# Optimization experiments

Hardware: AMD Instinct MI355X
Metric: run time of the kernel (lower is better)

Reference implementation:

```python
import jax, jax.numpy as jnp
import numpy as np

N, E, D, H, L = 50000, 800000, 256, 256, 40
HIDLAYERS = 3
NEG_SLOPE = 0.2  # PyG GATConv default leaky_relu slope


def _add_self_loops(edge_index, n):
    loop = jnp.arange(n, dtype=edge_index.dtype)
    src = jnp.concatenate([edge_index[0], loop])
    dst = jnp.concatenate([edge_index[1], loop])
    return src, dst


def gcn_conv(x, edge_index, W, b, n):
    # PyG GCNConv: add self-loops, symmetric deg^-1/2 normalization, linear, scatter-add
    src, dst = _add_self_loops(edge_index, n)
    ones = jnp.ones(src.shape[0], dtype=x.dtype)
    deg = jax.ops.segment_sum(ones, dst, num_segments=n)
    dinv = jnp.where(deg > 0, jax.lax.rsqrt(deg), 0.0)
    h = x @ W  # [n, out]
    norm = dinv[src] * dinv[dst]  # [E+n]
    out = jax.ops.segment_sum(h[src] * norm[:, None], dst, num_segments=n)
    return out + b


def gat_conv(x, edge_index, W, a_src, a_dst, b, n):
    # PyG GATConv (heads=1): add self-loops, e = leaky_relu(a_src.h_j + a_dst.h_i),
    # softmax over incoming edges per destination node, weighted scatter-add
    src, dst = _add_self_loops(edge_index, n)
    h = x @ W  # [n, H]
    al_src = h @ a_src  # [n]
    al_dst = h @ a_dst  # [n]
    e = jax.nn.leaky_relu(al_src[src] + al_dst[dst], NEG_SLOPE)  # [E+n]
    # numerically stable segment softmax over dst (self-loops => no empty segments)
    m = jax.ops.segment_max(e, dst, num_segments=n)
    ex = jnp.exp(e - m[dst])
    z = jax.ops.segment_sum(ex, dst, num_segments=n)
    alpha = ex / z[dst]
    out = jax.ops.segment_sum(h[src] * alpha[:, None], dst, num_segments=n)
    return out + b


def setup_inputs() -> dict:
    key = jax.random.key(0)
    ks = jax.random.split(key, 8)
    s = 0.05
    return {
        "x": jax.random.normal(ks[0], (N, D), jnp.float32),
        "edge_index": jax.random.randint(ks[1], (2, E), 0, N, dtype=jnp.int64),
        "W1": jax.random.normal(ks[2], (D, H), jnp.float32) * s,
        "b1": jnp.zeros((H,), jnp.float32),
        "Wg": jax.random.normal(ks[3], (H, H), jnp.float32) * s,
        "a_src": jax.random.normal(ks[4], (H,), jnp.float32) * s,
        "a_dst": jax.random.normal(ks[5], (H,), jnp.float32) * s,
        "bg": jnp.zeros((H,), jnp.float32),
        "W2": jax.random.normal(ks[6], (H, L), jnp.float32) * s,
        "b2": jnp.zeros((L,), jnp.float32),
    }


def reference(x, edge_index, W1, b1, Wg, a_src, a_dst, bg, W2, b2):
    n = x.shape[0]
    # feature standardization (torch .std is unbiased, ddof=1)
    x = (x - x.mean(axis=0, keepdims=True)) / x.std(axis=0, keepdims=True, ddof=1)
    x = jax.nn.relu(gcn_conv(x, edge_index, W1, b1, n))  # dropout = identity (eval)
    for _ in range(HIDLAYERS - 1):
        x = jax.nn.relu(gat_conv(x, edge_index, Wg, a_src, a_dst, bg, n))
    x = gcn_conv(x, edge_index, W2, b2, n)
    return jax.nn.log_softmax(x, axis=1)
```

## Files before the change

### kernel.cpp

```cpp
#include <hip/hip_runtime.h>
#include <math.h>

#define DD 256
#define LL 40
#define NSLOPE 0.2f
#define SCHUNK 1024

typedef unsigned short u16;
typedef unsigned int uint;
typedef __attribute__((ext_vector_type(8))) short short8;
typedef __attribute__((ext_vector_type(4))) float f32x4;

__device__ __forceinline__ float bf2f(u16 v) { return __uint_as_float(((uint)v) << 16); }
__device__ __forceinline__ u16 f2bf(float f) {
  uint u = __float_as_uint(f);
  return (u16)((u + 0x7fff + ((u >> 16) & 1)) >> 16);
}
__device__ __forceinline__ void acc8(float* a, uint4 v) {
  a[0] += __uint_as_float(v.x << 16);
  a[1] += __uint_as_float(v.x & 0xffff0000u);
  a[2] += __uint_as_float(v.y << 16);
  a[3] += __uint_as_float(v.y & 0xffff0000u);
  a[4] += __uint_as_float(v.z << 16);
  a[5] += __uint_as_float(v.z & 0xffff0000u);
  a[6] += __uint_as_float(v.w << 16);
  a[7] += __uint_as_float(v.w & 0xffff0000u);
}
__device__ __forceinline__ void wacc8(float* a, uint4 v, float w) {
  a[0] += w * __uint_as_float(v.x << 16);
  a[1] += w * __uint_as_float(v.x & 0xffff0000u);
  a[2] += w * __uint_as_float(v.y << 16);
  a[3] += w * __uint_as_float(v.y & 0xffff0000u);
  a[4] += w * __uint_as_float(v.z << 16);
  a[5] += w * __uint_as_float(v.z & 0xffff0000u);
  a[6] += w * __uint_as_float(v.w << 16);
  a[7] += w * __uint_as_float(v.w & 0xffff0000u);
}

__global__ __launch_bounds__(256) void k_colstats(const float* __restrict__ x, float* __restrict__ csum,
                                                  float* __restrict__ csq, int n, int rowsPerBlk) {
  int col = threadIdx.x;
  int r0 = blockIdx.x * rowsPerBlk;
  int r1 = min(r0 + rowsPerBlk, n);
  float s0 = 0.f, s1 = 0.f, s2 = 0.f, s3 = 0.f;
  float q0 = 0.f, q1 = 0.f, q2 = 0.f, q3 = 0.f;
  const float* xc = x + col;
  int r = r0;
  for (; r + 8 <= r1; r += 8) {
    float v0 = xc[(size_t)(r + 0) * DD];
    float v1 = xc[(size_t)(r + 1) * DD];
    float v2 = xc[(size_t)(r + 2) * DD];
    float v3 = xc[(size_t)(r + 3) * DD];
    float v4 = xc[(size_t)(r + 4) * DD];
    float v5 = xc[(size_t)(r + 5) * DD];
    float v6 = xc[(size_t)(r + 6) * DD];
    float v7 = xc[(size_t)(r + 7) * DD];
    s0 += v0; q0 = fmaf(v0, v0, q0);
    s1 += v1; q1 = fmaf(v1, v1, q1);
    s2 += v2; q2 = fmaf(v2, v2, q2);
    s3 += v3; q3 = fmaf(v3, v3, q3);
    s0 += v4; q0 = fmaf(v4, v4, q0);
    s1 += v5; q1 = fmaf(v5, v5, q1);
    s2 += v6; q2 = fmaf(v6, v6, q2);
    s3 += v7; q3 = fmaf(v7, v7, q3);
  }
  for (; r < r1; ++r) {
    float v = xc[(size_t)r * DD];
    s0 += v; q0 = fmaf(v, v, q0);
  }
  atomicAdd(&csum[col], (s0 + s1) + (s2 + s3));
  atomicAdd(&csq[col], (q0 + q1) + (q2 + q3));
}

__global__ void k_finalize_stats(const float* __restrict__ csum, const float* __restrict__ csq,
                                 float* __restrict__ mean, float* __restrict__ rstd, int n) {
  int j = threadIdx.x;
  float s = csum[j], q = csq[j];
  float m = s / (float)n;
  float var = (q - s * m) / (float)(n - 1);
  mean[j] = m;
  rstd[j] = 1.0f / sqrtf(var);
}

__global__ void k_standardize(const float* __restrict__ x, const float* __restrict__ mean,
                              const float* __restrict__ rstd, u16* __restrict__ xs, int total4) {
  int i = blockIdx.x * blockDim.x + threadIdx.x;
  if (i >= total4) return;
  int c4 = i & (DD / 4 - 1);
  float4 v = ((const float4*)x)[i];
  float4 m = ((const float4*)mean)[c4];
  float4 r = ((const float4*)rstd)[c4];
  uint2 o;
  o.x = (uint)f2bf((v.x - m.x) * r.x) | ((uint)f2bf((v.y - m.y) * r.y) << 16);
  o.y = (uint)f2bf((v.z - m.z) * r.z) | ((uint)f2bf((v.w - m.w) * r.w) << 16);
  ((uint2*)xs)[i] = o;
}

__global__ void k_convWt(const float* __restrict__ W, u16* __restrict__ Wt, int K, int N) {
  int k = blockIdx.x;
  for (int nn = threadIdx.x; nn < N; nn += blockDim.x)
    Wt[(size_t)nn * K + k] = f2bf(W[(size_t)k * N + nn]);
}

__global__ void k_count_deg(const int* __restrict__ edst, int E, int* __restrict__ degi) {
  int i = blockIdx.x * blockDim.x + threadIdx.x;
  if (i < E) atomicAdd(&degi[edst[i]], 1);
}

__global__ __launch_bounds__(256) void k_blocksum(const int* __restrict__ degi, int* __restrict__ bsum, int n) {
  int b = blockIdx.x, tid = threadIdx.x;
  int base = b * SCHUNK;
  int end = min(base + SCHUNK, n);
  int s = 0;
  for (int i = base + tid; i < end; i += 256) s += degi[i] + 1;
  __shared__ int ws[4];
  #pragma unroll
  for (int off = 32; off >= 1; off >>= 1) s += __shfl_down(s, off);
  if ((tid & 63) == 0) ws[tid >> 6] = s;
  __syncthreads();
  if (tid == 0) bsum[b] = ws[0] + ws[1] + ws[2] + ws[3];
}

__global__ void k_scan_bsums(int* __restrict__ bsum, int nb) {
  int lane = threadIdx.x;
  int orig = (lane < nb) ? bsum[lane] : 0;
  int v = orig;
  #pragma unroll
  for (int off = 1; off < 64; off <<= 1) {
    int t = __shfl_up(v, off);
    if (lane >= off) v += t;
  }
  if (lane < nb) bsum[lane] = v - orig;
}

__global__ __launch_bounds__(256) void k_rowptr_write(const int* __restrict__ degi, const int* __restrict__ bsum,
                                                      int* __restrict__ rowptr, int* __restrict__ cursor,
                                                      float* __restrict__ dinv, int n) {
  int b = blockIdx.x, tid = threadIdx.x;
  int base = b * SCHUNK + tid * 4;
  int d[4];
  int t = 0;
  #pragma unroll
  for (int j = 0; j < 4; ++j) {
    int i = base + j;
    d[j] = (i < n) ? degi[i] + 1 : 0;
    t += d[j];
  }
  __shared__ int sc[256];
  sc[tid] = t;
  __syncthreads();
  for (int off = 1; off < 256; off <<= 1) {
    int v = 0;
    if (tid >= off) v = sc[tid - off];
    __syncthreads();
    if (tid >= off) sc[tid] += v;
    __syncthreads();
  }
  int run = bsum[b] + sc[tid] - t;
  #pragma unroll
  for (int j = 0; j < 4; ++j) {
    int i = base + j;
    if (i < n) {
      rowptr[i] = run;
      cursor[i] = run;
      dinv[i] = rsqrtf((float)d[j]);
      run += d[j];
      if (i == n - 1) rowptr[n] = run;
    }
  }
}

__global__ void k_scatter(const int* __restrict__ esrc, const int* __restrict__ edst, int E,
                          int* __restrict__ cursor, int* __restrict__ csrsrc) {
  int i = blockIdx.x * blockDim.x + threadIdx.x;
  if (i < E) {
    int d = edst[i];
    int p = atomicAdd(&cursor[d], 1);
    csrsrc[p] = esrc[i];
  }
}

__global__ void k_selfloop(const int* __restrict__ rowptr, int* __restrict__ csrsrc, int n) {
  int i = blockIdx.x * blockDim.x + threadIdx.x;
  if (i < n) csrsrc[rowptr[i + 1] - 1] = i;
}

__global__ __launch_bounds__(256) void k_mfma_gemm128(const u16* __restrict__ A, const u16* __restrict__ Bt,
                                                      u16* __restrict__ C, int M, int N, int K,
                                                      const float* __restrict__ rowScale) {
  __shared__ u16 As[128 * 40];
  __shared__ u16 Bs[128 * 40];
  int tid = threadIdx.x;
  int wave = tid >> 6, lane = tid & 63, quad = lane >> 4, l16 = lane & 15;
  int rowBase = blockIdx.y * 128, colBase = blockIdx.x * 128;
  f32x4 acc[2][8] = {};
  for (int k0 = 0; k0 < K; k0 += 32) {
    #pragma unroll
    for (int i = 0; i < 2; ++i) {
      int ch = tid + i * 256;
      int r = ch >> 2, cc = (ch & 3) * 8;
      int gr = min(rowBase + r, M - 1);
      *(uint4*)&As[r * 40 + cc] = *(const uint4*)(A + (size_t)gr * K + k0 + cc);
      *(uint4*)&Bs[r * 40 + cc] = *(const uint4*)(Bt + (size_t)(colBase + r) * K + k0 + cc);
    }
    __syncthreads();
    short8 af0 = *(const short8*)&As[(wave * 32 + l16) * 40 + quad * 8];
    short8 af1 = *(const short8*)&As[(wave * 32 + 16 + l16) * 40 + quad * 8];
    #pragma unroll
    for (int j = 0; j < 8; ++j) {
      short8 bf = *(const short8*)&Bs[(j * 16 + l16) * 40 + quad * 8];
      acc[0][j] = __builtin_amdgcn_mfma_f32_16x16x32_bf16(af0, bf, acc[0][j], 0, 0, 0);
      acc[1][j] = __builtin_amdgcn_mfma_f32_16x16x32_bf16(af1, bf, acc[1][j], 0, 0, 0);
    }
    __syncthreads();
  }
  #pragma unroll
  for (int i = 0; i < 2; ++i) {
    #pragma unroll
    for (int r = 0; r < 4; ++r) {
      int gr = rowBase + wave * 32 + i * 16 + quad * 4 + r;
      if (gr >= M) continue;
      float sc = rowScale ? rowScale[gr] : 1.0f;
      #pragma unroll
      for (int j = 0; j < 8; ++j) {
        int gc = colBase + j * 16 + l16;
        C[(size_t)gr * N + gc] = f2bf(acc[i][j][r] * sc);
      }
    }
  }
}

__global__ __launch_bounds__(256) void k_mfma_gemm(const u16* __restrict__ A, const u16* __restrict__ Bt,
                                                   u16* __restrict__ C, int M, int N, int K,
                                                   const float* __restrict__ rowScale) {
  __shared__ u16 As[128 * 40];
  __shared__ u16 Bs[64 * 40];
  int tid = threadIdx.x;
  int wave = tid >> 6, lane = tid & 63, quad = lane >> 4, l16 = lane & 15;
  int rowBase = blockIdx.y * 128, colBase = blockIdx.x * 64;
  f32x4 acc[2][4] = {};
  for (int k0 = 0; k0 < K; k0 += 32) {
    #pragma unroll
    for (int i = 0; i < 2; ++i) {
      int ch = tid + i * 256;
      int r = ch >> 2, cc = (ch & 3) * 8;
      int gr = rowBase + r;
      uint4 v = make_uint4(0, 0, 0, 0);
      if (gr < M) v = *(const uint4*)(A + (size_t)gr * K + k0 + cc);
      *(uint4*)&As[r * 40 + cc] = v;
    }
    {
      int r = tid >> 2, cc = (tid & 3) * 8;
      int gn = colBase + r;
      uint4 v = make_uint4(0, 0, 0, 0);
      if (gn < N) v = *(const uint4*)(Bt + (size_t)gn * K + k0 + cc);
      *(uint4*)&Bs[r * 40 + cc] = v;
    }
    __syncthreads();
    short8 af[2];
    af[0] = *(const short8*)&As[(wave * 32 + l16) * 40 + quad * 8];
    af[1] = *(const short8*)&As[(wave * 32 + 16 + l16) * 40 + quad * 8];
    short8 bf[4];
    #pragma unroll
    for (int j = 0; j < 4; ++j) bf[j] = *(const short8*)&Bs[(j * 16 + l16) * 40 + quad * 8];
    #pragma unroll
    for (int i = 0; i < 2; ++i)
      #pragma unroll
      for (int j = 0; j < 4; ++j)
        acc[i][j] = __builtin_amdgcn_mfma_f32_16x16x32_bf16(af[i], bf[j], acc[i][j], 0, 0, 0);
    __syncthreads();
  }
  #pragma unroll
  for (int i = 0; i < 2; ++i) {
    #pragma unroll
    for (int r = 0; r < 4; ++r) {
      int gr = rowBase + wave * 32 + i * 16 + quad * 4 + r;
      if (gr >= M) continue;
      float sc = rowScale ? rowScale[gr] : 1.0f;
      #pragma unroll
      for (int j = 0; j < 4; ++j) {
        int gc = colBase + j * 16 + l16;
        if (gc < N) C[(size_t)gr * N + gc] = f2bf(acc[i][j][r] * sc);
      }
    }
  }
}

__global__ __launch_bounds__(256) void k_gcn_agg(const u16* __restrict__ hs, const int* __restrict__ rowptr,
                                                 const int* __restrict__ csrsrc, const float* __restrict__ dinv,
                                                 const float* __restrict__ bias, u16* __restrict__ out, int n) {
  int wave = (blockIdx.x * blockDim.x + threadIdx.x) >> 6;
  int lane = threadIdx.x & 63;
  int sub = lane >> 5, l = lane & 31;
  int w = wave * 2 + sub;
  if (w >= n) return;
  int p0 = rowptr[w], p1 = rowptr[w + 1];
  float a[8] = {};
  int p = p0;
  for (; p + 4 <= p1; p += 4) {
    int s0 = csrsrc[p], s1 = csrsrc[p + 1], s2 = csrsrc[p + 2], s3 = csrsrc[p + 3];
    uint4 v0 = *(const uint4*)(hs + (size_t)s0 * DD + l * 8);
    uint4 v1 = *(const uint4*)(hs + (size_t)s1 * DD + l * 8);
    uint4 v2 = *(const uint4*)(hs + (size_t)s2 * DD + l * 8);
    uint4 v3 = *(const uint4*)(hs + (size_t)s3 * DD + l * 8);
    acc8(a, v0); acc8(a, v1); acc8(a, v2); acc8(a, v3);
  }
  for (; p < p1; ++p) {
    int s = csrsrc[p];
    uint4 v = *(const uint4*)(hs + (size_t)s * DD + l * 8);
    acc8(a, v);
  }
  float dd = dinv[w];
  float4 b0 = ((const float4*)bias)[l * 2];
  float4 b1 = ((const float4*)bias)[l * 2 + 1];
  float r0 = fmaxf(dd * a[0] + b0.x, 0.f), r1 = fmaxf(dd * a[1] + b0.y, 0.f);
  float r2 = fmaxf(dd * a[2] + b0.z, 0.f), r3 = fmaxf(dd * a[3] + b0.w, 0.f);
  float r4 = fmaxf(dd * a[4] + b1.x, 0.f), r5 = fmaxf(dd * a[5] + b1.y, 0.f);
  float r6 = fmaxf(dd * a[6] + b1.z, 0.f), r7 = fmaxf(dd * a[7] + b1.w, 0.f);
  uint4 o;
  o.x = (uint)f2bf(r0) | ((uint)f2bf(r1) << 16);
  o.y = (uint)f2bf(r2) | ((uint)f2bf(r3) << 16);
  o.z = (uint)f2bf(r4) | ((uint)f2bf(r5) << 16);
  o.w = (uint)f2bf(r6) | ((uint)f2bf(r7) << 16);
  *(uint4*)(out + (size_t)w * DD + l * 8) = o;
}

__global__ __launch_bounds__(256) void k_al(const u16* __restrict__ h, const float* __restrict__ va,
                                            const float* __restrict__ vb, float* __restrict__ als,
                                            float* __restrict__ ald, int n) {
  int w = (blockIdx.x * blockDim.x + threadIdx.x) >> 6;
  int lane = threadIdx.x & 63;
  if (w >= n) return;
  uint2 v = *(const uint2*)(h + (size_t)w * DD + lane * 4);
  float x0 = __uint_as_float(v.x << 16), x1 = __uint_as_float(v.x & 0xffff0000u);
  float x2 = __uint_as_float(v.y << 16), x3 = __uint_as_float(v.y & 0xffff0000u);
  float4 a = ((const float4*)va)[lane];
  float4 b = ((const float4*)vb)[lane];
  float s1 = x0 * a.x + x1 * a.y + x2 * a.z + x3 * a.w;
  float s2 = x0 * b.x + x1 * b.y + x2 * b.z + x3 * b.w;
  #pragma unroll
  for (int off = 1; off < 64; off <<= 1) {
    s1 += __shfl_xor(s1, off);
    s2 += __shfl_xor(s2, off);
  }
  if (lane == 0) { als[w] = s1; ald[w] = s2; }
}

__global__ __launch_bounds__(256) void k_gat_agg(const u16* __restrict__ h, const int* __restrict__ rowptr,
                                                 const int* __restrict__ csrsrc, const float* __restrict__ als,
                                                 const float* __restrict__ ald, const float* __restrict__ bias,
                                                 u16* __restrict__ out, int n) {
  int wave = (blockIdx.x * blockDim.x + threadIdx.x) >> 6;
  int lane = threadIdx.x & 63;
  int sub = lane >> 5, l = lane & 31;
  int w = wave * 2 + sub;
  if (w >= n) return;
  float ad = ald[w];
  int p0 = rowptr[w], p1 = rowptr[w + 1];
  float m = -1e30f, z = 0.f;
  for (int p = p0 + l; p < p1; p += 32) {
    float e = als[csrsrc[p]] + ad;
    e = (e > 0.f) ? e : NSLOPE * e;
    if (e > m) { z = z * __expf(m - e) + 1.f; m = e; }
    else z += __expf(e - m);
  }
  #pragma unroll
  for (int off = 16; off >= 1; off >>= 1) {
    float m2 = __shfl_xor(m, off), z2 = __shfl_xor(z, off);
    float M = fmaxf(m, m2);
    z = z * __expf(m - M) + z2 * __expf(m2 - M);
    m = M;
  }
  float invz = 1.0f / z;
  float a[8] = {};
  int p = p0;
  for (; p + 4 <= p1; p += 4) {
    int s0 = csrsrc[p], s1 = csrsrc[p + 1], s2 = csrsrc[p + 2], s3 = csrsrc[p + 3];
    float e0 = als[s0] + ad; e0 = (e0 > 0.f) ? e0 : NSLOPE * e0;
    float e1 = als[s1] + ad; e1 = (e1 > 0.f) ? e1 : NSLOPE * e1;
    float e2 = als[s2] + ad; e2 = (e2 > 0.f) ? e2 : NSLOPE * e2;
    float e3 = als[s3] + ad; e3 = (e3 > 0.f) ? e3 : NSLOPE * e3;
    uint4 v0 = *(const uint4*)(h + (size_t)s0 * DD + l * 8);
    uint4 v1 = *(const uint4*)(h + (size_t)s1 * DD + l * 8);
    uint4 v2 = *(const uint4*)(h + (size_t)s2 * DD + l * 8);
    uint4 v3 = *(const uint4*)(h + (size_t)s3 * DD + l * 8);
    wacc8(a, v0, __expf(e0 - m) * invz);
    wacc8(a, v1, __expf(e1 - m) * invz);
    wacc8(a, v2, __expf(e2 - m) * invz);
    wacc8(a, v3, __expf(e3 - m) * invz);
  }
  for (; p < p1; ++p) {
    int s = csrsrc[p];
    float e = als[s] + ad; e = (e > 0.f) ? e : NSLOPE * e;
    uint4 v = *(const uint4*)(h + (size_t)s * DD + l * 8);
    wacc8(a, v, __expf(e - m) * invz);
  }
  float4 b0 = ((const float4*)bias)[l * 2];
  float4 b1 = ((const float4*)bias)[l * 2 + 1];
  float r0 = fmaxf(a[0] + b0.x, 0.f), r1 = fmaxf(a[1] + b0.y, 0.f);
  float r2 = fmaxf(a[2] + b0.z, 0.f), r3 = fmaxf(a[3] + b0.w, 0.f);
  float r4 = fmaxf(a[4] + b1.x, 0.f), r5 = fmaxf(a[5] + b1.y, 0.f);
  float r6 = fmaxf(a[6] + b1.z, 0.f), r7 = fmaxf(a[7] + b1.w, 0.f);
  uint4 o;
  o.x = (uint)f2bf(r0) | ((uint)f2bf(r1) << 16);
  o.y = (uint)f2bf(r2) | ((uint)f2bf(r3) << 16);
  o.z = (uint)f2bf(r4) | ((uint)f2bf(r5) << 16);
  o.w = (uint)f2bf(r6) | ((uint)f2bf(r7) << 16);
  *(uint4*)(out + (size_t)w * DD + l * 8) = o;
}

__global__ __launch_bounds__(256) void k_gcn2_lsm(const u16* __restrict__ hs, const int* __restrict__ rowptr,
                                                  const int* __restrict__ csrsrc, const float* __restrict__ dinv,
                                                  const float* __restrict__ bias, float* __restrict__ out, int n) {
  int w = (blockIdx.x * blockDim.x + threadIdx.x) >> 6;
  int lane = threadIdx.x & 63;
  if (w >= n) return;
  int p0 = rowptr[w], p1 = rowptr[w + 1];
  float acc = 0.f;
  int p = p0;
  for (; p + 4 <= p1; p += 4) {
    int s0 = csrsrc[p], s1 = csrsrc[p + 1], s2 = csrsrc[p + 2], s3 = csrsrc[p + 3];
    if (lane < LL) {
      float v0 = bf2f(hs[(size_t)s0 * LL + lane]);
      float v1 = bf2f(hs[(size_t)s1 * LL + lane]);
      float v2 = bf2f(hs[(size_t)s2 * LL + lane]);
      float v3 = bf2f(hs[(size_t)s3 * LL + lane]);
      acc += v0 + v1 + v2 + v3;
    }
  }
  for (; p < p1; ++p) {
    int s = csrsrc[p];
    if (lane < LL) acc += bf2f(hs[(size_t)s * LL + lane]);
  }
  float dd = dinv[w];
  float v = (lane < LL) ? dd * acc + bias[lane] : -INFINITY;
  float m = v;
  #pragma unroll
  for (int off = 1; off < 64; off <<= 1) m = fmaxf(m, __shfl_xor(m, off));
  float ex = (lane < LL) ? __expf(v - m) : 0.f;
  float z = ex;
  #pragma unroll
  for (int off = 1; off < 64; off <<= 1) z += __shfl_xor(z, off);
  if (lane < LL) out[(size_t)w * LL + lane] = v - m - logf(z);
}

extern "C" void kernel_launch(void* const* d_in, const int* in_sizes, int n_in,
                              void* d_out, int out_size, void* d_ws, size_t ws_size,
                              hipStream_t stream) {
  const float* x   = (const float*)d_in[0];
  const int*   ei  = (const int*)d_in[1];
  const float* W1  = (const float*)d_in[2];
  const float* b1  = (const float*)d_in[3];
  const float* Wg  = (const float*)d_in[4];
  const float* a_s = (const float*)d_in[5];
  const float* a_d = (const float*)d_in[6];
  const float* bg  = (const float*)d_in[7];
  const float* W2  = (const float*)d_in[8];
  const float* b2  = (const float*)d_in[9];
  float* out = (float*)d_out;

  const int n = in_sizes[0] / DD;
  const int E = in_sizes[1] / 2;
  const int M = E + n;
  const int* esrc = ei;
  const int* edst = ei + E;

  char* wp = (char*)d_ws;
  auto carve = [&](size_t bytes) -> char* {
    char* p = wp;
    wp += (bytes + 255) & ~(size_t)255;
    return p;
  };
  u16*   buf0   = (u16*)carve((size_t)n * DD * 2);
  u16*   buf1   = (u16*)carve((size_t)n * DD * 2);
  u16*   h40    = (u16*)carve((size_t)n * LL * 2);
  u16*   W1t    = (u16*)carve((size_t)DD * DD * 2);
  u16*   Wgt    = (u16*)carve((size_t)DD * DD * 2);
  u16*   W2t    = (u16*)carve((size_t)LL * DD * 2);
  int*   csrsrc = (int*)carve((size_t)M * 4);
  int*   rowptr = (int*)carve((size_t)(n + 1) * 4);
  int*   cursor = (int*)carve((size_t)n * 4);
  int*   degi   = (int*)carve((size_t)n * 4);
  int*   bsum   = (int*)carve(64 * 4);
  float* dinv   = (float*)carve((size_t)n * 4);
  float* alsA   = (float*)carve((size_t)n * 4);
  float* aldA   = (float*)carve((size_t)n * 4);
  float* csum   = (float*)carve(DD * 4);
  float* csq    = (float*)carve(DD * 4);
  float* mean   = (float*)carve(DD * 4);
  float* rstd   = (float*)carve(DD * 4);

  hipMemsetAsync(degi, 0, (size_t)n * 4, stream);
  hipMemsetAsync(csum, 0, DD * 4, stream);
  hipMemsetAsync(csq, 0, DD * 4, stream);

  const int rowsPerBlk = 32;
  k_colstats<<<(n + rowsPerBlk - 1) / rowsPerBlk, DD, 0, stream>>>(x, csum, csq, n, rowsPerBlk);
  k_finalize_stats<<<1, DD, 0, stream>>>(csum, csq, mean, rstd, n);
  int total4 = n * (DD / 4);
  k_standardize<<<(total4 + 255) / 256, 256, 0, stream>>>(x, mean, rstd, buf0, total4);

  k_convWt<<<DD, 256, 0, stream>>>(W1, W1t, DD, DD);
  k_convWt<<<DD, 256, 0, stream>>>(Wg, Wgt, DD, DD);
  k_convWt<<<DD, 64, 0, stream>>>(W2, W2t, DD, LL);

  int nb = (n + SCHUNK - 1) / SCHUNK;
  k_count_deg<<<(E + 255) / 256, 256, 0, stream>>>(edst, E, degi);
  k_blocksum<<<nb, 256, 0, stream>>>(degi, bsum, n);
  k_scan_bsums<<<1, 64, 0, stream>>>(bsum, nb);
  k_rowptr_write<<<nb, 256, 0, stream>>>(degi, bsum, rowptr, cursor, dinv, n);
  k_scatter<<<(E + 255) / 256, 256, 0, stream>>>(esrc, edst, E, cursor, csrsrc);
  k_selfloop<<<(n + 255) / 256, 256, 0, stream>>>(rowptr, csrsrc, n);

  dim3 blk(256);
  dim3 gemmGrid(DD / 128, (n + 127) / 128);
  int aggGrid1 = (n + 3) / 4;
  int aggGrid2 = (n + 7) / 8;

  k_mfma_gemm128<<<gemmGrid, blk, 0, stream>>>(buf0, W1t, buf1, n, DD, DD, dinv);
  k_gcn_agg<<<aggGrid2, blk, 0, stream>>>(buf1, rowptr, csrsrc, dinv, b1, buf0, n);

  for (int l = 0; l < 2; ++l) {
    k_mfma_gemm128<<<gemmGrid, blk, 0, stream>>>(buf0, Wgt, buf1, n, DD, DD, nullptr);
    k_al<<<aggGrid1, blk, 0, stream>>>(buf1, a_s, a_d, alsA, aldA, n);
    k_gat_agg<<<aggGrid2, blk, 0, stream>>>(buf1, rowptr, csrsrc, alsA, aldA, bg, buf0, n);
  }

  dim3 gemmGrid2(1, (n + 127) / 128);
  k_mfma_gemm<<<gemmGrid2, blk, 0, stream>>>(buf0, W2t, h40, n, LL, DD, dinv);
  k_gcn2_lsm<<<aggGrid1, blk, 0, stream>>>(h40, rowptr, csrsrc, dinv, b2, out, n);
}
```

Before: 568.0 us.

## Merge preprocessing kernels and fuse GAT attention logits into GEMM epilogue

Independent preprocessing kernels (column stats, degree count, weight transposes; stats finalize and block sums; standardize and rowptr write) are merged into three multi-role kernels to cut launch count. The self-loop write moves into the rowptr kernel, with each self-loop placed at the head of its row and the cursor starting one past it. The separate attention-logit kernel is removed: the GEMM epilogue computes per-row dot products with a_src/a_dst from fp32 accumulators and atomically adds the partials from the two column blocks into zeroed buffers. This adds extra memsets and float atomics, which make summation order nondeterministic, and the logits now come from unrounded fp32 values instead of bf16 h.

```diff
diff --git a/kernel.cpp b/kernel.cpp
--- a/kernel.cpp
+++ b/kernel.cpp
@@ -37,88 +37,86 @@
   a[7] += w * __uint_as_float(v.w & 0xffff0000u);
 }
 
-__global__ __launch_bounds__(256) void k_colstats(const float* __restrict__ x, float* __restrict__ csum,
-                                                  float* __restrict__ csq, int n, int rowsPerBlk) {
-  int col = threadIdx.x;
-  int r0 = blockIdx.x * rowsPerBlk;
-  int r1 = min(r0 + rowsPerBlk, n);
-  float s0 = 0.f, s1 = 0.f, s2 = 0.f, s3 = 0.f;
-  float q0 = 0.f, q1 = 0.f, q2 = 0.f, q3 = 0.f;
-  const float* xc = x + col;
-  int r = r0;
-  for (; r + 8 <= r1; r += 8) {
-    float v0 = xc[(size_t)(r + 0) * DD];
-    float v1 = xc[(size_t)(r + 1) * DD];
-    float v2 = xc[(size_t)(r + 2) * DD];
-    float v3 = xc[(size_t)(r + 3) * DD];
-    float v4 = xc[(size_t)(r + 4) * DD];
-    float v5 = xc[(size_t)(r + 5) * DD];
-    float v6 = xc[(size_t)(r + 6) * DD];
-    float v7 = xc[(size_t)(r + 7) * DD];
-    s0 += v0; q0 = fmaf(v0, v0, q0);
-    s1 += v1; q1 = fmaf(v1, v1, q1);
-    s2 += v2; q2 = fmaf(v2, v2, q2);
-    s3 += v3; q3 = fmaf(v3, v3, q3);
-    s0 += v4; q0 = fmaf(v4, v4, q0);
-    s1 += v5; q1 = fmaf(v5, v5, q1);
-    s2 += v6; q2 = fmaf(v6, v6, q2);
-    s3 += v7; q3 = fmaf(v7, v7, q3);
-  }
-  for (; r < r1; ++r) {
-    float v = xc[(size_t)r * DD];
-    s0 += v; q0 = fmaf(v, v, q0);
-  }
-  atomicAdd(&csum[col], (s0 + s1) + (s2 + s3));
-  atomicAdd(&csq[col], (q0 + q1) + (q2 + q3));
-}
-
-__global__ void k_finalize_stats(const float* __restrict__ csum, const float* __restrict__ csq,
-                                 float* __restrict__ mean, float* __restrict__ rstd, int n) {
-  int j = threadIdx.x;
-  float s = csum[j], q = csq[j];
-  float m = s / (float)n;
-  float var = (q - s * m) / (float)(n - 1);
-  mean[j] = m;
-  rstd[j] = 1.0f / sqrtf(var);
-}
-
-__global__ void k_standardize(const float* __restrict__ x, const float* __restrict__ mean,
-                              const float* __restrict__ rstd, u16* __restrict__ xs, int total4) {
-  int i = blockIdx.x * blockDim.x + threadIdx.x;
-  if (i >= total4) return;
-  int c4 = i & (DD / 4 - 1);
-  float4 v = ((const float4*)x)[i];
-  float4 m = ((const float4*)mean)[c4];
-  float4 r = ((const float4*)rstd)[c4];
-  uint2 o;
-  o.x = (uint)f2bf((v.x - m.x) * r.x) | ((uint)f2bf((v.y - m.y) * r.y) << 16);
-  o.y = (uint)f2bf((v.z - m.z) * r.z) | ((uint)f2bf((v.w - m.w) * r.w) << 16);
-  ((uint2*)xs)[i] = o;
-}
-
-__global__ void k_convWt(const float* __restrict__ W, u16* __restrict__ Wt, int K, int N) {
-  int k = blockIdx.x;
-  for (int nn = threadIdx.x; nn < N; nn += blockDim.x)
-    Wt[(size_t)nn * K + k] = f2bf(W[(size_t)k * N + nn]);
-}
-
-__global__ void k_count_deg(const int* __restrict__ edst, int E, int* __restrict__ degi) {
-  int i = blockIdx.x * blockDim.x + threadIdx.x;
-  if (i < E) atomicAdd(&degi[edst[i]], 1);
-}
-
-__global__ __launch_bounds__(256) void k_blocksum(const int* __restrict__ degi, int* __restrict__ bsum, int n) {
-  int b = blockIdx.x, tid = threadIdx.x;
-  int base = b * SCHUNK;
-  int end = min(base + SCHUNK, n);
-  int s = 0;
-  for (int i = base + tid; i < end; i += 256) s += degi[i] + 1;
-  __shared__ int ws[4];
-  #pragma unroll
-  for (int off = 32; off >= 1; off >>= 1) s += __shfl_down(s, off);
-  if ((tid & 63) == 0) ws[tid >> 6] = s;
-  __syncthreads();
-  if (tid == 0) bsum[b] = ws[0] + ws[1] + ws[2] + ws[3];
+__global__ __launch_bounds__(256) void k_pre1(const float* __restrict__ x, float* __restrict__ csum,
+                                              float* __restrict__ csq, int n, int rowsPerBlk, int nbC,
+                                              const int* __restrict__ edst, int E, int* __restrict__ degi, int nbE,
+                                              const float* __restrict__ W1, u16* __restrict__ W1t,
+                                              const float* __restrict__ Wg, u16* __restrict__ Wgt,
+                                              const float* __restrict__ W2, u16* __restrict__ W2t) {
+  int b = blockIdx.x;
+  int tid = threadIdx.x;
+  if (b < nbC) {
+    int r0 = b * rowsPerBlk;
+    int r1 = min(r0 + rowsPerBlk, n);
+    float s0 = 0.f, s1 = 0.f, s2 = 0.f, s3 = 0.f;
+    float q0 = 0.f, q1 = 0.f, q2 = 0.f, q3 = 0.f;
+    const float* xc = x + tid;
+    int r = r0;
+    for (; r + 8 <= r1; r += 8) {
+      float v0 = xc[(size_t)(r + 0) * DD];
+      float v1 = xc[(size_t)(r + 1) * DD];
+      float v2 = xc[(size_t)(r + 2) * DD];
+      float v3 = xc[(size_t)(r + 3) * DD];
+      float v4 = xc[(size_t)(r + 4) * DD];
+      float v5 = xc[(size_t)(r + 5) * DD];
+      float v6 = xc[(size_t)(r + 6) * DD];
+      float v7 = xc[(size_t)(r + 7) * DD];
+      s0 += v0; q0 = fmaf(v0, v0, q0);
+      s1 += v1; q1 = fmaf(v1, v1, q1);
+      s2 += v2; q2 = fmaf(v2, v2, q2);
+      s3 += v3; q3 = fmaf(v3, v3, q3);
+      s0 += v4; q0 = fmaf(v4, v4, q0);
+      s1 += v5; q1 = fmaf(v5, v5, q1);
+      s2 += v6; q2 = fmaf(v6, v6, q2);
+      s3 += v7; q3 = fmaf(v7, v7, q3);
+    }
+    for (; r < r1; ++r) {
+      float v = xc[(size_t)r * DD];
+      s0 += v; q0 = fmaf(v, v, q0);
+    }
+    atomicAdd(&csum[tid], (s0 + s1) + (s2 + s3));
+    atomicAdd(&csq[tid], (q0 + q1) + (q2 + q3));
+  } else if (b < nbC + nbE) {
+    int i = (b - nbC) * 256 + tid;
+    if (i < E) atomicAdd(&degi[edst[i]], 1);
+  } else {
+    int b2 = b - nbC - nbE;
+    if (b2 < DD) {
+      int k = b2;
+      for (int nn = tid; nn < DD; nn += 256) W1t[(size_t)nn * DD + k] = f2bf(W1[(size_t)k * DD + nn]);
+    } else if (b2 < 2 * DD) {
+      int k = b2 - DD;
+      for (int nn = tid; nn < DD; nn += 256) Wgt[(size_t)nn * DD + k] = f2bf(Wg[(size_t)k * DD + nn]);
+    } else {
+      int k = b2 - 2 * DD;
+      for (int nn = tid; nn < LL; nn += 256) W2t[(size_t)nn * DD + k] = f2bf(W2[(size_t)k * LL + nn]);
+    }
+  }
+}
+
+__global__ __launch_bounds__(256) void k_pre2(const float* __restrict__ csum, const float* __restrict__ csq,
+                                              float* __restrict__ mean, float* __restrict__ rstd, int n,
+                                              const int* __restrict__ degi, int* __restrict__ bsum, int nb) {
+  int b = blockIdx.x;
+  int tid = threadIdx.x;
+  if (b == nb) {
+    float s = csum[tid], q = csq[tid];
+    float m = s / (float)n;
+    float var = (q - s * m) / (float)(n - 1);
+    mean[tid] = m;
+    rstd[tid] = 1.0f / sqrtf(var);
+  } else {
+    int base = b * SCHUNK;
+    int end = min(base + SCHUNK, n);
+    int s = 0;
+    for (int i = base + tid; i < end; i += 256) s += degi[i] + 1;
+    __shared__ int ws[4];
+    #pragma unroll
+    for (int off = 32; off >= 1; off >>= 1) s += __shfl_down(s, off);
+    if ((tid & 63) == 0) ws[tid >> 6] = s;
+    __syncthreads();
+    if (tid == 0) bsum[b] = ws[0] + ws[1] + ws[2] + ws[3];
+  }
 }
 
 __global__ void k_scan_bsums(int* __restrict__ bsum, int nb) {
@@ -133,39 +131,58 @@
   if (lane < nb) bsum[lane] = v - orig;
 }
 
-__global__ __launch_bounds__(256) void k_rowptr_write(const int* __restrict__ degi, const int* __restrict__ bsum,
-                                                      int* __restrict__ rowptr, int* __restrict__ cursor,
-                                                      float* __restrict__ dinv, int n) {
-  int b = blockIdx.x, tid = threadIdx.x;
-  int base = b * SCHUNK + tid * 4;
-  int d[4];
-  int t = 0;
-  #pragma unroll
-  for (int j = 0; j < 4; ++j) {
-    int i = base + j;
-    d[j] = (i < n) ? degi[i] + 1 : 0;
-    t += d[j];
-  }
-  __shared__ int sc[256];
-  sc[tid] = t;
-  __syncthreads();
-  for (int off = 1; off < 256; off <<= 1) {
-    int v = 0;
-    if (tid >= off) v = sc[tid - off];
+__global__ __launch_bounds__(256) void k_pre4(const float* __restrict__ x, const float* __restrict__ mean,
+                                              const float* __restrict__ rstd, u16* __restrict__ xs,
+                                              int total4, int nbS,
+                                              const int* __restrict__ degi, const int* __restrict__ bsum,
+                                              int* __restrict__ rowptr, int* __restrict__ cursor,
+                                              int* __restrict__ csrsrc, float* __restrict__ dinv, int n) {
+  int b = blockIdx.x;
+  int tid = threadIdx.x;
+  if (b < nbS) {
+    int i = b * 256 + tid;
+    if (i >= total4) return;
+    int c4 = i & (DD / 4 - 1);
+    float4 v = ((const float4*)x)[i];
+    float4 m = ((const float4*)mean)[c4];
+    float4 r = ((const float4*)rstd)[c4];
+    uint2 o;
+    o.x = (uint)f2bf((v.x - m.x) * r.x) | ((uint)f2bf((v.y - m.y) * r.y) << 16);
+    o.y = (uint)f2bf((v.z - m.z) * r.z) | ((uint)f2bf((v.w - m.w) * r.w) << 16);
+    ((uint2*)xs)[i] = o;
+  } else {
+    int bb = b - nbS;
+    int base = bb * SCHUNK + tid * 4;
+    int d[4];
+    int t = 0;
+    #pragma unroll
+    for (int j = 0; j < 4; ++j) {
+      int i = base + j;
+      d[j] = (i < n) ? degi[i] + 1 : 0;
+      t += d[j];
+    }
+    __shared__ int sc[256];
+    sc[tid] = t;
     __syncthreads();
-    if (tid >= off) sc[tid] += v;
-    __syncthreads();
-  }
-  int run = bsum[b] + sc[tid] - t;
-  #pragma unroll
-  for (int j = 0; j < 4; ++j) {
-    int i = base + j;
-    if (i < n) {
-      rowptr[i] = run;
-      cursor[i] = run;
-      dinv[i] = rsqrtf((float)d[j]);
-      run += d[j];
-      if (i == n - 1) rowptr[n] = run;
+    for (int off = 1; off < 256; off <<= 1) {
+      int v = 0;
+      if (tid >= off) v = sc[tid - off];
+      __syncthreads();
+      if (tid >= off) sc[tid] += v;
+      __syncthreads();
+    }
+    int run = bsum[bb] + sc[tid] - t;
+    #pragma unroll
+    for (int j = 0; j < 4; ++j) {
+      int i = base + j;
+      if (i < n) {
+        rowptr[i] = run;
+        csrsrc[run] = i;
+        cursor[i] = run + 1;
+        dinv[i] = rsqrtf((float)d[j]);
+        run += d[j];
+        if (i == n - 1) rowptr[n] = run;
+      }
     }
   }
 }
@@ -180,14 +197,11 @@
   }
 }
 
-__global__ void k_selfloop(const int* __restrict__ rowptr, int* __restrict__ csrsrc, int n) {
-  int i = blockIdx.x * blockDim.x + threadIdx.x;
-  if (i < n) csrsrc[rowptr[i + 1] - 1] = i;
-}
-
 __global__ __launch_bounds__(256) void k_mfma_gemm128(const u16* __restrict__ A, const u16* __restrict__ Bt,
                                                       u16* __restrict__ C, int M, int N, int K,
-                                                      const float* __restrict__ rowScale) {
+                                                      const float* __restrict__ rowScale,
+                                                      const float* __restrict__ aS, const float* __restrict__ aD,
+                                                      float* __restrict__ als, float* __restrict__ ald) {
   __shared__ u16 As[128 * 40];
   __shared__ u16 Bs[128 * 40];
   int tid = threadIdx.x;
@@ -225,6 +239,25 @@
       for (int j = 0; j < 8; ++j) {
         int gc = colBase + j * 16 + l16;
         C[(size_t)gr * N + gc] = f2bf(acc[i][j][r] * sc);
+      }
+      if (aS) {
+        float t1 = 0.f, t2 = 0.f;
+        #pragma unroll
+        for (int j = 0; j < 8; ++j) {
+          int gc = colBase + j * 16 + l16;
+          float v = acc[i][j][r];
+          t1 = fmaf(v, aS[gc], t1);
+          t2 = fmaf(v, aD[gc], t2);
+        }
+        #pragma unroll
+        for (int off = 1; off < 16; off <<= 1) {
+          t1 += __shfl_xor(t1, off);
+          t2 += __shfl_xor(t2, off);
+        }
+        if (l16 == 0) {
+          atomicAdd(&als[gr], t1);
+          atomicAdd(&ald[gr], t2);
+        }
       }
     }
   }
@@ -323,27 +356,6 @@
   o.z = (uint)f2bf(r4) | ((uint)f2bf(r5) << 16);
   o.w = (uint)f2bf(r6) | ((uint)f2bf(r7) << 16);
   *(uint4*)(out + (size_t)w * DD + l * 8) = o;
-}
-
-__global__ __launch_bounds__(256) void k_al(const u16* __restrict__ h, const float* __restrict__ va,
-                                            const float* __restrict__ vb, float* __restrict__ als,
-                                            float* __restrict__ ald, int n) {
-  int w = (blockIdx.x * blockDim.x + threadIdx.x) >> 6;
-  int lane = threadIdx.x & 63;
-  if (w >= n) return;
-  uint2 v = *(const uint2*)(h + (size_t)w * DD + lane * 4);
-  float x0 = __uint_as_float(v.x << 16), x1 = __uint_as_float(v.x & 0xffff0000u);
-  float x2 = __uint_as_float(v.y << 16), x3 = __uint_as_float(v.y & 0xffff0000u);
-  float4 a = ((const float4*)va)[lane];
-  float4 b = ((const float4*)vb)[lane];
-  float s1 = x0 * a.x + x1 * a.y + x2 * a.z + x3 * a.w;
-  float s2 = x0 * b.x + x1 * b.y + x2 * b.z + x3 * b.w;
-  #pragma unroll
-  for (int off = 1; off < 64; off <<= 1) {
-    s1 += __shfl_xor(s1, off);
-    s2 += __shfl_xor(s2, off);
-  }
-  if (lane == 0) { als[w] = s1; ald[w] = s2; }
 }
 
 __global__ __launch_bounds__(256) void k_gat_agg(const u16* __restrict__ h, const int* __restrict__ rowptr,
@@ -485,6 +497,8 @@
   float* dinv   = (float*)carve((size_t)n * 4);
   float* alsA   = (float*)carve((size_t)n * 4);
   float* aldA   = (float*)carve((size_t)n * 4);
+  float* alsB   = (float*)carve((size_t)n * 4);
+  float* aldB   = (float*)carve((size_t)n * 4);
   float* csum   = (float*)carve(DD * 4);
   float* csq    = (float*)carve(DD * 4);
   float* mean   = (float*)carve(DD * 4);
@@ -493,38 +507,41 @@
   hipMemsetAsync(degi, 0, (size_t)n * 4, stream);
   hipMemsetAsync(csum, 0, DD * 4, stream);
   hipMemsetAsync(csq, 0, DD * 4, stream);
+  hipMemsetAsync(alsA, 0, (size_t)n * 4, stream);
+  hipMemsetAsync(aldA, 0, (size_t)n * 4, stream);
+  hipMemsetAsync(alsB, 0, (size_t)n * 4, stream);
+  hipMemsetAsync(aldB, 0, (size_t)n * 4, stream);
 
   const int rowsPerBlk = 32;
-  k_colstats<<<(n + rowsPerBlk - 1) / rowsPerBlk, DD, 0, stream>>>(x, csum, csq, n, rowsPerBlk);
-  k_finalize_stats<<<1, DD, 0, stream>>>(csum, csq, mean, rstd, n);
+  int nbC = (n + rowsPerBlk - 1) / rowsPerBlk;
+  int nbE = (E + 255) / 256;
+  int nb  = (n + SCHUNK - 1) / SCHUNK;
   int total4 = n * (DD / 4);
-  k_standardize<<<(total4 + 255) / 256, 256, 0, stream>>>(x, mean, rstd, buf0, total4);
-
-  k_convWt<<<DD, 256, 0, stream>>>(W1, W1t, DD, DD);
-  k_convWt<<<DD, 256, 0, stream>>>(Wg, Wgt, DD, DD);
-  k_convWt<<<DD, 64, 0, stream>>>(W2, W2t, DD, LL);
-
-  int nb = (n + SCHUNK - 1) / SCHUNK;
-  k_count_deg<<<(E + 255) / 256, 256, 0, stream>>>(edst, E, degi);
-  k_blocksum<<<nb, 256, 0, stream>>>(degi, bsum, n);
+  int nbS = (total4 + 255) / 256;
+  k_pre1<<<nbC + nbE + 3 * DD, 256, 0, stream>>>(x, csum, csq, n, rowsPerBlk, nbC,
+                                                 edst, E, degi, nbE, W1, W1t, Wg, Wgt, W2, W2t);
+  k_pre2<<<nb + 1, 256, 0, stream>>>(csum, csq, mean, rstd, n, degi, bsum, nb);
   k_scan_bsums<<<1, 64, 0, stream>>>(bsum, nb);
-  k_rowptr_write<<<nb, 256, 0, stream>>>(degi, bsum, rowptr, cursor, dinv, n);
+  k_pre4<<<nbS + nb, 256, 0, stream>>>(x, mean, rstd, buf0, total4, nbS,
+                                       degi, bsum, rowptr, cursor, csrsrc, dinv, n);
   k_scatter<<<(E + 255) / 256, 256, 0, stream>>>(esrc, edst, E, cursor, csrsrc);
-  k_selfloop<<<(n + 255) / 256, 256, 0, stream>>>(rowptr, csrsrc, n);
 
   dim3 blk(256);
   dim3 gemmGrid(DD / 128, (n + 127) / 128);
   int aggGrid1 = (n + 3) / 4;
   int aggGrid2 = (n + 7) / 8;
 
-  k_mfma_gemm128<<<gemmGrid, blk, 0, stream>>>(buf0, W1t, buf1, n, DD, DD, dinv);
+  k_mfma_gemm128<<<gemmGrid, blk, 0, stream>>>(buf0, W1t, buf1, n, DD, DD, dinv,
+                                               nullptr, nullptr, nullptr, nullptr);
   k_gcn_agg<<<aggGrid2, blk, 0, stream>>>(buf1, rowptr, csrsrc, dinv, b1, buf0, n);
 
-  for (int l = 0; l < 2; ++l) {
-    k_mfma_gemm128<<<gemmGrid, blk, 0, stream>>>(buf0, Wgt, buf1, n, DD, DD, nullptr);
-    k_al<<<aggGrid1, blk, 0, stream>>>(buf1, a_s, a_d, alsA, aldA, n);
-    k_gat_agg<<<aggGrid2, blk, 0, stream>>>(buf1, rowptr, csrsrc, alsA, aldA, bg, buf0, n);
-  }
+  k_mfma_gemm128<<<gemmGrid, blk, 0, stream>>>(buf0, Wgt, buf1, n, DD, DD, nullptr,
+                                               a_s, a_d, alsA, aldA);
+  k_gat_agg<<<aggGrid2, blk, 0, stream>>>(buf1, rowptr, csrsrc, alsA, aldA, bg, buf0, n);
+
+  k_mfma_gemm128<<<gemmGrid, blk, 0, stream>>>(buf0, Wgt, buf1, n, DD, DD, nullptr,
+                                               a_s, a_d, alsB, aldB);
+  k_gat_agg<<<aggGrid2, blk, 0, stream>>>(buf1, rowptr, csrsrc, alsB, aldB, bg, buf0, n);
 
   dim3 gemmGrid2(1, (n + 127) / 128);
   k_mfma_gemm<<<gemmGrid2, blk, 0, stream>>>(buf0, W2t, h40, n, LL, DD, dinv);
```

Result: faster. 556.6 us (-2.0%).
